# Performance work log

Measured on AMD Instinct MI355X. Metric: run time of the kernel, lower is better.

Reference implementation:

```python
import jax, jax.numpy as jnp
import numpy as np

B, N, F, K, H = 2, 1024, 64, 8, 4
M1 = K + 1                # 9
M2 = (F - 1) * K + 1      # 505
TEMP = 1.0


def setup_inputs() -> dict:
    key = jax.random.key(0)
    ks = jax.random.split(key, 8)
    x = jax.random.normal(ks[0], (B, N, F), dtype=jnp.float32)
    # Bernoulli(0.05) dense adjacency
    adj = (jax.random.uniform(ks[1], (B, N, N)) < 0.05).astype(jnp.float32)
    mask = jnp.ones((B, N), dtype=jnp.float32)
    Wl = jax.random.normal(ks[2], (F, K * H), dtype=jnp.float32) * 0.05
    bl = jnp.zeros((K * H,), dtype=jnp.float32)
    Wr = jax.random.normal(ks[3], (F, K * H), dtype=jnp.float32) * 0.05
    br = jnp.zeros((K * H,), dtype=jnp.float32)
    # fixed affine layer: y = x @ aff_w + aff_b, aff_w[:, :F] = -I, aff_b[M2] = 1
    aff_w = jnp.zeros((F, M1 * M2), dtype=jnp.float32).at[:, :F].set(-jnp.eye(F, dtype=jnp.float32))
    aff_b = jnp.zeros((M1 * M2,), dtype=jnp.float32).at[M2].set(1.0)
    Wm = jax.random.normal(ks[4], (M1 * M2, F), dtype=jnp.float32) * 0.02
    bm = jnp.zeros((F,), dtype=jnp.float32)
    return dict(x=x, adj=adj, mask=mask, Wl=Wl, bl=bl, Wr=Wr, br=br,
                aff_w=aff_w, aff_b=aff_b, Wm=Wm, bm=bm)


def reference(x, adj, mask, Wl, bl, Wr, br, aff_w, aff_b, Wm, bm):
    # --- multi-head edge attention ---
    x_l = (x @ Wl + bl).reshape(B, N, K, H)   # [B,N,K,H]
    x_r = (x @ Wr + br).reshape(B, N, K, H)
    # scores[b,i,j,n,g] = leaky_relu(x_l[b,j] + x_r[b,i]) / temp
    scores = jax.nn.leaky_relu(x_l[:, None, :, :, :] + x_r[:, :, None, :, :]) / TEMP  # [B,N,N,K,H]
    attn_mask = mask[:, None, :] * mask[:, :, None]                # [B,N,N]
    scores = jnp.where(attn_mask[..., None, None] == 0, -1e9, scores)
    att = jax.nn.softmax(scores, axis=2)                           # softmax over source nodes j
    att = jnp.maximum(att * adj[..., None, None], 1e-6)            # clamp(min=1e-6) STE trick
    att = att / jnp.sum(att, axis=2, keepdims=True)                # renormalize
    # --- attention-weighted neighbor gather ---
    x_h = x.reshape(B, N, H, F // H)
    agg = jnp.einsum('bjgk,bijng->bingk', x_h, att).reshape(B, N, K, F)  # [B,N,K,F]
    # --- fixed affine + FFT log-domain geometric mean ---
    x_aff = (agg @ aff_w + aff_b).reshape(B, N, K, M1, M2)
    x_fft = jnp.fft.fft2(x_aff)                                    # over (M1,M2)
    mag = jnp.exp(jnp.mean(jnp.log(jnp.abs(x_fft) + 1e-6), axis=2))  # [B,N,M1,M2]
    ang = jnp.sum(jnp.angle(x_fft), axis=2)
    x_agg = jnp.fft.ifft2(mag * jnp.exp(1j * ang)).real.reshape(B, N, M1 * M2)
    # --- output MLP + node mask ---
    out = x_agg @ Wm + bm
    return out * mask[..., None]
```

## Files before the change

### kernel.cpp

```cpp
#include <hip/hip_runtime.h>
#include <math.h>

#define NN 1024
#define FD 64
#define CH 32
#define M1D 9
#define M2D 505
#define QH 253
#define THALF 2273
#define KPAD 4608
#define KSPLIT 16
#define KCHUNK 288
#define G1SZ 291456
#define G1KS 8

#define FSQRT(x) __builtin_amdgcn_sqrtf(x)
#define FRCP(x)  __builtin_amdgcn_rcpf(x)

typedef short short8 __attribute__((ext_vector_type(8)));
typedef float f32x4 __attribute__((ext_vector_type(4)));

__device__ __forceinline__ unsigned short f2bf(float x) {
    unsigned int u = __builtin_bit_cast(unsigned int, x);
    return (unsigned short)((u + 0x7FFFu + ((u >> 16) & 1u)) >> 16);
}

#define OFF_SUMXP 1024
#define OFF_GMT   4096
#define OFF_XL    151552
#define OFF_XR    217088
#define OFF_AGG   282624
#define OFF_Y     1331200
#define OFF_G1P   6049792

__global__ __launch_bounds__(256) void fused_pre_kernel(
    const float* __restrict__ x,
    const float* __restrict__ Wl, const float* __restrict__ bl,
    const float* __restrict__ Wr, const float* __restrict__ br,
    const float* __restrict__ Wm, const float* __restrict__ bm,
    const float* __restrict__ mask,
    float* __restrict__ xl, float* __restrict__ xr,
    float* __restrict__ sumxp, float* __restrict__ G1p,
    float* __restrict__ out)
{
    __shared__ float As[64][68];
    __shared__ float Bs[64][64];
    int bid = blockIdx.x, tid = threadIdx.x;

    if (bid < 576) {
        int mt = bid & 7, m1 = (bid >> 3) % 9, ks = bid / 72;
        int r0 = mt * 64, k0 = ks * 64;
        const float* Wmb = Wm + (size_t)m1 * M2D * FD;
        float ra[16], rb[16];
        #pragma unroll
        for (int i = 0; i < 16; i++) {
            int l = tid + i*256;
            int r = l >> 6, k = l & 63;
            int rr = r0 + r, m2 = k0 + k;
            float v = 0.f;
            if (rr < 506 && m2 < M2D) {
                int q = rr >> 1;
                int t = (q * m2) % M2D;
                float ang = (float)t * (-6.2831853f / 505.0f);
                float s, c; __sincosf(ang, &s, &c);
                v = (rr & 1) ? -s : c;
            }
            ra[i] = v;
        }
        #pragma unroll
        for (int i = 0; i < 16; i++) {
            int l = tid + i*256;
            int k = l >> 6, f = l & 63;
            int krow = k0 + k;
            rb[i] = (krow < M2D) ? Wmb[(size_t)krow*FD + f] : 0.f;
        }
        #pragma unroll
        for (int i = 0; i < 16; i++) {
            int l = tid + i*256;
            As[l & 63][l >> 6] = ra[i];
        }
        #pragma unroll
        for (int i = 0; i < 16; i++) {
            int l = tid + i*256;
            Bs[l >> 6][l & 63] = rb[i];
        }
        __syncthreads();
        float acc[4][4] = {{0.f}};
        int tm = (tid >> 4) * 4, tf = (tid & 15) * 4;
        #pragma unroll 8
        for (int k = 0; k < 64; k++) {
            float4 a = *(const float4*)&As[k][tm];
            float4 b = *(const float4*)&Bs[k][tf];
            acc[0][0] += a.x*b.x; acc[0][1] += a.x*b.y; acc[0][2] += a.x*b.z; acc[0][3] += a.x*b.w;
            acc[1][0] += a.y*b.x; acc[1][1] += a.y*b.y; acc[1][2] += a.y*b.z; acc[1][3] += a.y*b.w;
            acc[2][0] += a.z*b.x; acc[2][1] += a.z*b.y; acc[2][2] += a.z*b.z; acc[2][3] += a.z*b.w;
            acc[3][0] += a.w*b.x; acc[3][1] += a.w*b.y; acc[3][2] += a.w*b.z; acc[3][3] += a.w*b.w;
        }
        float* G1k = G1p + (size_t)ks * G1SZ;
        #pragma unroll
        for (int i = 0; i < 4; i++) {
            int r = r0 + tm + i;
            if (r >= 506) continue;
            int q = r >> 1, reim = r & 1;
            size_t base = (size_t)(m1*QH + q) * 128;
            #pragma unroll
            for (int j = 0; j < 4; j++)
                G1k[base + (tf + j)*2 + reim] = acc[i][j];
        }
    } else if (bid < 1088) {
        int grp = tid >> 6, lt = tid & 63;
        int node = (bid - 576)*4 + grp;
        float* xrow = &As[0][0] + grp*FD;
        xrow[lt] = x[(size_t)node*FD + lt];
        __syncthreads();
        int c = lt & 31;
        const float* W = (lt < 32) ? Wl : Wr;
        float acc = (lt < 32) ? bl[c] : br[c];
        #pragma unroll
        for (int f = 0; f < FD; f++) acc += xrow[f] * W[f*CH + c];
        float* dst = (lt < 32) ? xl : xr;
        dst[(size_t)node*CH + c] = acc;
    } else if (bid < 1096) {
        int bb = (bid - 1088)*4 + (tid >> 6);
        int f = tid & 63;
        int b = bb >> 4, chunk = bb & 15;
        const float* xb = x + (size_t)b * NN * FD;
        float acc = 0.f;
        int j0 = chunk * 64;
        #pragma unroll 4
        for (int j = j0; j < j0 + 64; j++) acc += xb[j*FD + f];
        sumxp[bb*64 + f] = acc;
    } else {
        int idx = (bid - 1096)*256 + tid;
        float4 bv = ((const float4*)bm)[idx & 15];
        float mk = mask[idx >> 4];
        bv.x *= mk; bv.y *= mk; bv.z *= mk; bv.w *= mk;
        ((float4*)out)[idx] = bv;
    }
}

__global__ __launch_bounds__(256) void fused_mid_kernel(
    const float* __restrict__ x, const float* __restrict__ adj,
    const float* __restrict__ xl, const float* __restrict__ xr,
    const float* __restrict__ sumxp, const float* __restrict__ G1p,
    float* __restrict__ agg, unsigned short* __restrict__ GmT)
{
    int bid = blockIdx.x, tid = threadIdx.x;

    if (bid >= 2048) {
        __shared__ float wps[18];
        if (tid < 9) {
            float s, c; __sincosf((float)tid * (-6.2831853f / 9.0f), &s, &c);
            wps[2*tid] = c; wps[2*tid+1] = s;
        }
        __syncthreads();
        int t = (bid - 2048)*4 + (tid >> 6);
        int f = tid & 63;
        if (t >= THALF) {
            *(unsigned int*)&GmT[(size_t)f*KPAD + 2*t] = 0u;
            return;
        }
        int p, q;
        if (t < QH) { p = 0; q = t; }
        else { int u = t - QH; p = 1 + u / M2D; q = u % M2D; }
        int qq = (q < QH) ? q : (M2D - q);
        float sgn = (q < QH) ? 1.f : -1.f;
        float gr = 0.f, gi = 0.f;
        #pragma unroll
        for (int m1 = 0; m1 < M1D; m1++) {
            size_t o = ((size_t)(m1*QH + qq)*FD + f)*2;
            float ar = 0.f, ai = 0.f;
            #pragma unroll
            for (int ks = 0; ks < G1KS; ks++) {
                ar += G1p[(size_t)ks*G1SZ + o];
                ai += G1p[(size_t)ks*G1SZ + o + 1];
            }
            ai *= sgn;
            int pm = (p * m1) % M1D;
            float cr = wps[2*pm], ci = -wps[2*pm+1];
            gr += ar*cr - ai*ci;
            gi += ar*ci + ai*cr;
        }
        float scale = (t == 0) ? (1.0f/4545.0f) : (2.0f/4545.0f);
        unsigned int pk = (unsigned int)f2bf(gr*scale) | ((unsigned int)f2bf(-gi*scale) << 16);
        *(unsigned int*)&GmT[(size_t)f*KPAD + 2*t] = pk;
        return;
    }

    int node = bid;
    int b = node >> 10;
    __shared__ float xr_s[CH], Zinv[CH], Sinv[CH];
    __shared__ float red16[16][CH];
    __shared__ int act_list[NN + 8];
    __shared__ int act_n;
    __shared__ float qv2[64][CH];

    if (tid < CH) xr_s[tid] = xr[(size_t)node*CH + tid];
    if (tid == 0) act_n = 0;
    __syncthreads();

    int c = tid & 31, jl = tid >> 5;
    const float* xlb = xl + ((size_t)b << 10) * CH;
    const float* adjrow = adj + (size_t)node * NN;

    int c2 = tid & 15, jl16 = tid >> 4;
    const float2* xlb2 = (const float2*)xlb;
    float xrcx = xr_s[2*c2], xrcy = xr_s[2*c2+1];
    float zx = 0.f, zy = 0.f;
    for (int j0 = jl16; j0 < NN; j0 += 128) {
        float2 sv[8];
        #pragma unroll
        for (int u = 0; u < 8; u++) sv[u] = xlb2[(size_t)(j0 + u*16)*16 + c2];
        #pragma unroll
        for (int u = 0; u < 8; u++) {
            float s0 = sv[u].x + xrcx; s0 = s0 > 0.f ? s0 : 0.01f * s0;
            float s1 = sv[u].y + xrcy; s1 = s1 > 0.f ? s1 : 0.01f * s1;
            zx += __expf(s0); zy += __expf(s1);
        }
    }
    red16[jl16][2*c2]   = zx;
    red16[jl16][2*c2+1] = zy;

    float av[4];
    #pragma unroll
    for (int u = 0; u < 4; u++) av[u] = adjrow[tid + u*256];
    __syncthreads();
    if (tid < CH) {
        float z = 0.f;
        #pragma unroll
        for (int r = 0; r < 16; r++) z += red16[r][tid];
        Zinv[tid] = FRCP(z);
    }
    #pragma unroll
    for (int u = 0; u < 4; u++)
        if (av[u] != 0.f) { int p = atomicAdd(&act_n, 1); act_list[p] = tid + u*256; }
    __syncthreads();
    int nact = act_n;

    int f = tid & 63, n0 = tid >> 6;
    int g = f >> 4;
    int c0 = n0*4 + g, c1 = (n0+4)*4 + g;
    const float* xb = x + ((size_t)b << 10) * FD;
    float acc0 = 0.f, acc1 = 0.f, sacc = 0.f;

    for (int base = 0; base < nact; base += 64) {
        int cnt = min(64, nact - base);
        int cntp = (cnt + 7) & ~7;
        for (int u = tid; u < (cnt << 5); u += 256) {
            int jj = u >> 5, cc = u & 31;
            int j = act_list[base + jj];
            float s = xlb[j*CH + cc] + xr_s[cc];
            s = s > 0.f ? s : 0.01f * s;
            float pv = __expf(s) * Zinv[cc];
            float qq = fmaxf(pv, 1e-6f) - 1e-6f;
            qv2[jj][cc] = qq;
            sacc += qq;
        }
        for (int u = tid + (cnt << 5); u < (cntp << 5); u += 256)
            qv2[u >> 5][u & 31] = 0.f;
        if (tid < cntp - cnt) act_list[base + cnt + tid] = act_list[base];
        __syncthreads();
        for (int jb = 0; jb < cntp; jb += 8) {
            float xv[8];
            #pragma unroll
            for (int u = 0; u < 8; u++) xv[u] = xb[act_list[base + jb + u]*FD + f];
            #pragma unroll
            for (int u = 0; u < 8; u++) {
                acc0 += qv2[jb+u][c0] * xv[u];
                acc1 += qv2[jb+u][c1] * xv[u];
            }
        }
        __syncthreads();
    }
    red16[jl][c] = sacc;
    __syncthreads();
    if (tid < CH) {
        float s = 0.f;
        #pragma unroll
        for (int r = 0; r < 8; r++) s += red16[r][tid];
        Sinv[tid] = FRCP(s + (float)NN * 1e-6f);
    }
    __syncthreads();
    float sx = 0.f;
    #pragma unroll
    for (int cchunk = 0; cchunk < 16; cchunk++) sx += sumxp[(b*16 + cchunk)*64 + f];
    sx *= 1e-6f;
    agg[(size_t)node*512 + n0*FD + f]       = (acc0 + sx) * Sinv[c0];
    agg[(size_t)node*512 + (n0+4)*FD + f]   = (acc1 + sx) * Sinv[c1];
}

__global__ __launch_bounds__(256) void ay_kernel(const float* __restrict__ agg,
                                                 unsigned short* __restrict__ Yb) {
    int slab = blockIdx.x, nt = blockIdx.y;
    int tid = threadIdx.x;
    __shared__ float As2[64][68];
    __shared__ float Bs[64][64];
    int tm = (tid >> 4) * 4, tf = (tid & 15) * 4;
    float ra[16], rb[16];
    #pragma unroll
    for (int i = 0; i < 16; i++) {
        int l = tid + i*256;
        int r = l >> 6, k = l & 63;
        ra[i] = agg[(size_t)(slab*64 + r)*64 + k];
    }
    #pragma unroll
    for (int i = 0; i < 16; i++) {
        int l = tid + i*256;
        int k = l >> 6, cc = l & 63;
        int col = nt*64 + cc;
        float v = 0.f;
        if (col < 506) {
            int q = col >> 1;
            int tt = (q * k) % M2D;
            float ang = (float)tt * (-6.2831853f / 505.0f);
            float s, c; __sincosf(ang, &s, &c);
            v = (col & 1) ? s : c;
        }
        rb[i] = v;
    }
    #pragma unroll
    for (int i = 0; i < 16; i++) { int l = tid + i*256; As2[l & 63][l >> 6] = ra[i]; }
    #pragma unroll
    for (int i = 0; i < 16; i++) { int l = tid + i*256; Bs[l >> 6][l & 63] = rb[i]; }
    __syncthreads();
    float acc[4][4] = {{0.f}};
    #pragma unroll 8
    for (int k = 0; k < 64; k++) {
        float4 a = *(const float4*)&As2[k][tm];
        float4 b = *(const float4*)&Bs[k][tf];
        acc[0][0] += a.x*b.x; acc[0][1] += a.x*b.y; acc[0][2] += a.x*b.z; acc[0][3] += a.x*b.w;
        acc[1][0] += a.y*b.x; acc[1][1] += a.y*b.y; acc[1][2] += a.y*b.z; acc[1][3] += a.y*b.w;
        acc[2][0] += a.z*b.x; acc[2][1] += a.z*b.y; acc[2][2] += a.z*b.z; acc[2][3] += a.z*b.w;
        acc[3][0] += a.w*b.x; acc[3][1] += a.w*b.y; acc[3][2] += a.w*b.z; acc[3][3] += a.w*b.w;
    }
    __syncthreads();
    #pragma unroll
    for (int i = 0; i < 4; i++)
        #pragma unroll
        for (int j = 0; j < 4; j++)
            As2[tm + i][tf + j] = acc[i][j];
    __syncthreads();

    int qloc = tid & 31, node = tid >> 5;
    unsigned short* Yrow = Yb + (size_t)(slab*8 + node)*KPAD;
    int q = nt*32 + qloc;

    if (q <= 252) {
        float2 Av[8];
        #pragma unroll
        for (int n = 0; n < 8; n++)
            Av[n] = make_float2(As2[node*8 + n][2*qloc], As2[node*8 + n][2*qloc + 1]);

        const float CPt[5] = {1.0f, 0.766044443119f, 0.173648177667f, -0.5f, -0.939692620786f};
        const float SPt[5] = {0.0f, -0.642787609687f, -0.984807753012f, -0.866025403784f, -0.342020143326f};

        #define Y_PROD(CSIGN, TIDX)                                            \
        {                                                                      \
            float Pr = 1.f, Pi = 0.f, rp2 = 1.f;                               \
            _Pragma("unroll")                                                  \
            for (int n = 0; n < 8; n++) {                                      \
                float Xr = cp - Av[n].x, Xi = sp - (CSIGN) * Av[n].y;          \
                rp2 *= (Xr*Xr + Xi*Xi);                                        \
                float nPr = Pr*Xr - Pi*Xi;                                     \
                Pi = Pr*Xi + Pi*Xr; Pr = nPr;                                  \
            }                                                                  \
            float pAbs = FSQRT(Pr*Pr + Pi*Pi);                                 \
            float rp8 = FSQRT(FSQRT(FSQRT(FSQRT(rp2))));                       \
            float s = rp8 * FRCP(fmaxf(pAbs, 1e-20f));                         \
            unsigned int pk = (unsigned int)f2bf(s*Pr) | ((unsigned int)f2bf(s*Pi) << 16); \
            *(unsigned int*)&Yrow[2*(TIDX)] = pk;                              \
        }

        #pragma unroll
        for (int p = 0; p < 5; p++) {
            float cp = CPt[p], sp = SPt[p];
            int tfwd = (p == 0) ? q : (QH + (p-1)*M2D + q);
            Y_PROD(1.f, tfwd);
            if (p >= 1 && q >= 1) {
                int tmir = QH + (p-1)*M2D + (M2D - q);
                Y_PROD(-1.f, tmir);
            }
        }
        #undef Y_PROD
    }
    if (nt == 7 && tid < 248) {
        int rr = tid / 31, cc2 = tid % 31;
        unsigned short* Yr2 = Yb + (size_t)(slab*8 + rr)*KPAD;
        *(unsigned int*)&Yr2[2*THALF + 2*cc2] = 0u;
    }
}

__global__ __launch_bounds__(256) void gemm_kernel(const unsigned short* __restrict__ Yb,
                                                   const unsigned short* __restrict__ GmT,
                                                   const float* __restrict__ mask,
                                                   float* __restrict__ out) {
    int mtile = blockIdx.x, kc = blockIdx.y;
    int tid = threadIdx.x;
    __shared__ unsigned short Ys[64*40];
    __shared__ unsigned short Gs[64*40];
    int m0 = mtile * 64;
    int k0 = kc * KCHUNK;
    int r = tid >> 2, kg = (tid & 3) * 8;
    const unsigned short* Ysrc = Yb + (size_t)(m0 + r)*KPAD + k0 + kg;
    const unsigned short* Gsrc = GmT + (size_t)r*KPAD + k0 + kg;
    uint4 ya = *(const uint4*)Ysrc;
    uint4 ga = *(const uint4*)Gsrc;
    int w = tid >> 6, lane = tid & 63;
    int lm = lane & 15, quad = lane >> 4;
    f32x4 acc0 = {0.f,0.f,0.f,0.f}, acc1 = acc0, acc2 = acc0, acc3 = acc0;
    for (int ks = 0; ks < KCHUNK; ks += 32) {
        *(uint4*)&Ys[r*40 + kg] = ya;
        *(uint4*)&Gs[r*40 + kg] = ga;
        __syncthreads();
        if (ks + 32 < KCHUNK) {
            ya = *(const uint4*)(Ysrc + ks + 32);
            ga = *(const uint4*)(Gsrc + ks + 32);
        }
        short8 b  = *(const short8*)&Gs[(w*16 + lm)*40 + quad*8];
        short8 a0 = *(const short8*)&Ys[(lm)*40      + quad*8];
        short8 a1 = *(const short8*)&Ys[(16 + lm)*40 + quad*8];
        short8 a2 = *(const short8*)&Ys[(32 + lm)*40 + quad*8];
        short8 a3 = *(const short8*)&Ys[(48 + lm)*40 + quad*8];
        acc0 = __builtin_amdgcn_mfma_f32_16x16x32_bf16(a0, b, acc0, 0, 0, 0);
        acc1 = __builtin_amdgcn_mfma_f32_16x16x32_bf16(a1, b, acc1, 0, 0, 0);
        acc2 = __builtin_amdgcn_mfma_f32_16x16x32_bf16(a2, b, acc2, 0, 0, 0);
        acc3 = __builtin_amdgcn_mfma_f32_16x16x32_bf16(a3, b, acc3, 0, 0, 0);
        __syncthreads();
    }
    int col = w*16 + lm;
    #pragma unroll
    for (int rr = 0; rr < 4; rr++) {
        int row = m0 + quad*4 + rr;
        atomicAdd(&out[(size_t)row*FD + col],        acc0[rr] * mask[row]);
        atomicAdd(&out[(size_t)(row+16)*FD + col],   acc1[rr] * mask[row+16]);
        atomicAdd(&out[(size_t)(row+32)*FD + col],   acc2[rr] * mask[row+32]);
        atomicAdd(&out[(size_t)(row+48)*FD + col],   acc3[rr] * mask[row+48]);
    }
}

extern "C" void kernel_launch(void* const* d_in, const int* in_sizes, int n_in,
                              void* d_out, int out_size, void* d_ws, size_t ws_size,
                              hipStream_t stream) {
    const float* x    = (const float*)d_in[0];
    const float* adj  = (const float*)d_in[1];
    const float* mask = (const float*)d_in[2];
    const float* Wl   = (const float*)d_in[3];
    const float* bl   = (const float*)d_in[4];
    const float* Wr   = (const float*)d_in[5];
    const float* br   = (const float*)d_in[6];
    const float* Wm   = (const float*)d_in[9];
    const float* bm   = (const float*)d_in[10];
    float* out = (float*)d_out;
    float* ws  = (float*)d_ws;

    float* sumxp = ws + OFF_SUMXP;
    unsigned short* GmT = (unsigned short*)(ws + OFF_GMT);
    float* xl   = ws + OFF_XL;
    float* xr   = ws + OFF_XR;
    float* agg  = ws + OFF_AGG;
    unsigned short* Yb = (unsigned short*)(ws + OFF_Y);
    float* G1p  = ws + OFF_G1P;

    hipLaunchKernelGGL(fused_pre_kernel, dim3(1224), dim3(256), 0, stream,
                       x, Wl, bl, Wr, br, Wm, bm, mask, xl, xr, sumxp, G1p, out);
    hipLaunchKernelGGL(fused_mid_kernel, dim3(2624), dim3(256), 0, stream,
                       x, adj, xl, xr, sumxp, G1p, agg, GmT);
    hipLaunchKernelGGL(ay_kernel, dim3(256, 8), dim3(256), 0, stream, agg, Yb);
    hipLaunchKernelGGL(gemm_kernel, dim3(32, KSPLIT), dim3(256), 0, stream, Yb, GmT, mask, out);
}
```

Baseline: 168.5 us.

## Precompute DFT twiddle table once and share G1 partial loads across frequency rows

```diff
diff --git a/kernel.cpp b/kernel.cpp
--- a/kernel.cpp
+++ b/kernel.cpp
@@ -32,6 +32,7 @@
 #define OFF_AGG   282624
 #define OFF_Y     1331200
 #define OFF_G1P   6049792
+#define OFF_WT    8381440
 
 __global__ __launch_bounds__(256) void fused_pre_kernel(
     const float* __restrict__ x,
@@ -41,7 +42,7 @@
     const float* __restrict__ mask,
     float* __restrict__ xl, float* __restrict__ xr,
     float* __restrict__ sumxp, float* __restrict__ G1p,
-    float* __restrict__ out)
+    float* __restrict__ Wt, float* __restrict__ out)
 {
     __shared__ float As[64][68];
     __shared__ float Bs[64][64];
@@ -102,10 +103,10 @@
             int r = r0 + tm + i;
             if (r >= 506) continue;
             int q = r >> 1, reim = r & 1;
-            size_t base = (size_t)(m1*QH + q) * 128;
+            size_t base = (size_t)(m1*QH + q) * 128 + reim*64;
             #pragma unroll
             for (int j = 0; j < 4; j++)
-                G1k[base + (tf + j)*2 + reim] = acc[i][j];
+                G1k[base + tf + j] = acc[i][j];
         }
     } else if (bid < 1088) {
         int grp = tid >> 6, lt = tid & 63;
@@ -130,12 +131,24 @@
         #pragma unroll 4
         for (int j = j0; j < j0 + 64; j++) acc += xb[j*FD + f];
         sumxp[bb*64 + f] = acc;
-    } else {
+    } else if (bid < 1224) {
         int idx = (bid - 1096)*256 + tid;
         float4 bv = ((const float4*)bm)[idx & 15];
         float mk = mask[idx >> 4];
         bv.x *= mk; bv.y *= mk; bv.z *= mk; bv.w *= mk;
         ((float4*)out)[idx] = bv;
+    } else {
+        int idx = (bid - 1224)*256 + tid;
+        int m = idx >> 9, col = idx & 511;
+        float v = 0.f;
+        if (col < 506) {
+            int q = col >> 1;
+            int t = (q * m) % M2D;
+            float ang = (float)t * (-6.2831853f / 505.0f);
+            float s, c; __sincosf(ang, &s, &c);
+            v = (col & 1) ? s : c;
+        }
+        Wt[idx] = v;
     }
 }
 
@@ -148,42 +161,67 @@
     int bid = blockIdx.x, tid = threadIdx.x;
 
     if (bid >= 2048) {
+        int bid2 = bid - 2048;
+        if (bid2 == 64) {
+            for (int i = tid; i < 31*64; i += 256) {
+                int t = THALF + (i >> 6), f = i & 63;
+                *(unsigned int*)&GmT[(size_t)f*KPAD + 2*t] = 0u;
+            }
+            return;
+        }
         __shared__ float wps[18];
         if (tid < 9) {
             float s, c; __sincosf((float)tid * (-6.2831853f / 9.0f), &s, &c);
             wps[2*tid] = c; wps[2*tid+1] = s;
         }
         __syncthreads();
-        int t = (bid - 2048)*4 + (tid >> 6);
+        int qq = bid2*4 + (tid >> 6);
         int f = tid & 63;
-        if (t >= THALF) {
-            *(unsigned int*)&GmT[(size_t)f*KPAD + 2*t] = 0u;
-            return;
-        }
-        int p, q;
-        if (t < QH) { p = 0; q = t; }
-        else { int u = t - QH; p = 1 + u / M2D; q = u % M2D; }
-        int qq = (q < QH) ? q : (M2D - q);
-        float sgn = (q < QH) ? 1.f : -1.f;
-        float gr = 0.f, gi = 0.f;
+        if (qq >= QH) return;
+        float ar[M1D], ai[M1D];
         #pragma unroll
         for (int m1 = 0; m1 < M1D; m1++) {
-            size_t o = ((size_t)(m1*QH + qq)*FD + f)*2;
-            float ar = 0.f, ai = 0.f;
+            size_t o = (size_t)(m1*QH + qq) * 128 + f;
+            float sr = 0.f, si = 0.f;
             #pragma unroll
             for (int ks = 0; ks < G1KS; ks++) {
-                ar += G1p[(size_t)ks*G1SZ + o];
-                ai += G1p[(size_t)ks*G1SZ + o + 1];
-            }
-            ai *= sgn;
-            int pm = (p * m1) % M1D;
-            float cr = wps[2*pm], ci = -wps[2*pm+1];
-            gr += ar*cr - ai*ci;
-            gi += ar*ci + ai*cr;
-        }
-        float scale = (t == 0) ? (1.0f/4545.0f) : (2.0f/4545.0f);
-        unsigned int pk = (unsigned int)f2bf(gr*scale) | ((unsigned int)f2bf(-gi*scale) << 16);
-        *(unsigned int*)&GmT[(size_t)f*KPAD + 2*t] = pk;
+                sr += G1p[(size_t)ks*G1SZ + o];
+                si += G1p[(size_t)ks*G1SZ + o + 64];
+            }
+            ar[m1] = sr; ai[m1] = si;
+        }
+        #pragma unroll
+        for (int p = 0; p < 5; p++) {
+            {
+                int t = (p == 0) ? qq : (QH + (p-1)*M2D + qq);
+                float gr = 0.f, gi = 0.f;
+                #pragma unroll
+                for (int m1 = 0; m1 < M1D; m1++) {
+                    int pm = (p * m1) % M1D;
+                    float cr = wps[2*pm], ci = -wps[2*pm+1];
+                    gr += ar[m1]*cr - ai[m1]*ci;
+                    gi += ar[m1]*ci + ai[m1]*cr;
+                }
+                float scale = (t == 0) ? (1.0f/4545.0f) : (2.0f/4545.0f);
+                unsigned int pk = (unsigned int)f2bf(gr*scale) | ((unsigned int)f2bf(-gi*scale) << 16);
+                *(unsigned int*)&GmT[(size_t)f*KPAD + 2*t] = pk;
+            }
+            if (p >= 1 && qq >= 1) {
+                int t = QH + (p-1)*M2D + (M2D - qq);
+                float gr = 0.f, gi = 0.f;
+                #pragma unroll
+                for (int m1 = 0; m1 < M1D; m1++) {
+                    int pm = (p * m1) % M1D;
+                    float cr = wps[2*pm], ci = -wps[2*pm+1];
+                    float aim = -ai[m1];
+                    gr += ar[m1]*cr - aim*ci;
+                    gi += ar[m1]*ci + aim*cr;
+                }
+                float scale = 2.0f/4545.0f;
+                unsigned int pk = (unsigned int)f2bf(gr*scale) | ((unsigned int)f2bf(-gi*scale) << 16);
+                *(unsigned int*)&GmT[(size_t)f*KPAD + 2*t] = pk;
+            }
+        }
         return;
     }
 
@@ -290,6 +328,7 @@
 }
 
 __global__ __launch_bounds__(256) void ay_kernel(const float* __restrict__ agg,
+                                                 const float* __restrict__ Wt,
                                                  unsigned short* __restrict__ Yb) {
     int slab = blockIdx.x, nt = blockIdx.y;
     int tid = threadIdx.x;
@@ -306,17 +345,7 @@
     #pragma unroll
     for (int i = 0; i < 16; i++) {
         int l = tid + i*256;
-        int k = l >> 6, cc = l & 63;
-        int col = nt*64 + cc;
-        float v = 0.f;
-        if (col < 506) {
-            int q = col >> 1;
-            int tt = (q * k) % M2D;
-            float ang = (float)tt * (-6.2831853f / 505.0f);
-            float s, c; __sincosf(ang, &s, &c);
-            v = (col & 1) ? s : c;
-        }
-        rb[i] = v;
+        rb[i] = Wt[(size_t)(l >> 6)*512 + nt*64 + (l & 63)];
     }
     #pragma unroll
     for (int i = 0; i < 16; i++) { int l = tid + i*256; As2[l & 63][l >> 6] = ra[i]; }
@@ -460,11 +489,12 @@
     float* agg  = ws + OFF_AGG;
     unsigned short* Yb = (unsigned short*)(ws + OFF_Y);
     float* G1p  = ws + OFF_G1P;
-
-    hipLaunchKernelGGL(fused_pre_kernel, dim3(1224), dim3(256), 0, stream,
-                       x, Wl, bl, Wr, br, Wm, bm, mask, xl, xr, sumxp, G1p, out);
-    hipLaunchKernelGGL(fused_mid_kernel, dim3(2624), dim3(256), 0, stream,
+    float* Wt   = ws + OFF_WT;
+
+    hipLaunchKernelGGL(fused_pre_kernel, dim3(1352), dim3(256), 0, stream,
+                       x, Wl, bl, Wr, br, Wm, bm, mask, xl, xr, sumxp, G1p, Wt, out);
+    hipLaunchKernelGGL(fused_mid_kernel, dim3(2113), dim3(256), 0, stream,
                        x, adj, xl, xr, sumxp, G1p, agg, GmT);
-    hipLaunchKernelGGL(ay_kernel, dim3(256, 8), dim3(256), 0, stream, agg, Yb);
+    hipLaunchKernelGGL(ay_kernel, dim3(256, 8), dim3(256), 0, stream, agg, Wt, Yb);
     hipLaunchKernelGGL(gemm_kernel, dim3(32, KSPLIT), dim3(256), 0, stream, Yb, GmT, mask, out);
 }
```

Result: faster. 159.6 us (-5.3%).
